# Performance work log

Measured on AMD Instinct MI355X. Metric: run time of the kernel, lower is better.

## Reference

```python
import jax, jax.numpy as jnp
import numpy as np

B, S, D_IN, D_OUT = 4, 4096, 2048, 2048


def setup_inputs() -> dict:
    key = jax.random.key(0)
    kx, kw = jax.random.split(key)
    x = jax.random.normal(kx, (B, S, D_IN), dtype=jnp.float32)
    weight = jax.random.normal(kw, (D_OUT, D_IN), dtype=jnp.float32) * 0.02
    return {"x": x, "weight": weight}


def reference(x, weight):
    # Per-row absmax int8 activation quantization
    x_scale = jnp.clip(jnp.max(jnp.abs(x), axis=-1, keepdims=True), 1e-05, None)  # [B,S,1]
    x_quant = jnp.clip(jnp.round(x / x_scale * 127.0), -128.0, 127.0)
    # Ternary weight quantization (mean-centered absmean scale)
    w_mean = jnp.mean(weight)
    w_centered = weight - w_mean
    w_scale = jnp.clip(jnp.mean(jnp.abs(w_centered)), 1e-05, None)
    w_quant = jnp.clip(jnp.round(w_centered / w_scale), -1.0, 1.0)
    # GEMM on quantized values, then dequant rescale
    y = jnp.einsum('bsi,oi->bso', x_quant, w_quant)  # [B,S,D_OUT]
    y = y * (w_scale * x_scale / 127.0)
    return y.astype(x.dtype)
```

## Files before the change

### kernel.cpp

```cpp
#include <hip/hip_runtime.h>
#include <stdint.h>

#define M_TOT 16384
#define K_DIM 2048
#define N_DIM 2048
#define W_ELEMS (N_DIM * K_DIM)

typedef int v4i __attribute__((ext_vector_type(4)));

__device__ __forceinline__ void async_load16(const void* gptr, void* lptr) {
    __builtin_amdgcn_global_load_lds(
        (__attribute__((address_space(1))) void*)(uintptr_t)gptr,
        (__attribute__((address_space(3))) void*)(uint32_t)(uintptr_t)lptr,
        16, 0, 0);
}

__global__ void wsum_kernel(const float* __restrict__ w, double* __restrict__ sums) {
    int tid = blockIdx.x * 256 + threadIdx.x;
    const float4* w4 = (const float4*)w;
    double s = 0.0;
    for (int i = tid; i < W_ELEMS / 4; i += 512 * 256) {
        float4 v = w4[i];
        s += (double)v.x + (double)v.y + (double)v.z + (double)v.w;
    }
    #pragma unroll
    for (int off = 32; off; off >>= 1) s += __shfl_down(s, off);
    __shared__ double ls[4];
    if ((threadIdx.x & 63) == 0) ls[threadIdx.x >> 6] = s;
    __syncthreads();
    if (threadIdx.x == 0) atomicAdd(&sums[0], ls[0] + ls[1] + ls[2] + ls[3]);
}

__global__ void wabs_kernel(const float* __restrict__ w, double* __restrict__ sums) {
    double mean = sums[0] * (1.0 / (double)W_ELEMS);
    int tid = blockIdx.x * 256 + threadIdx.x;
    const float4* w4 = (const float4*)w;
    double s = 0.0;
    for (int i = tid; i < W_ELEMS / 4; i += 512 * 256) {
        float4 v = w4[i];
        s += fabs((double)v.x - mean) + fabs((double)v.y - mean) +
             fabs((double)v.z - mean) + fabs((double)v.w - mean);
    }
    #pragma unroll
    for (int off = 32; off; off >>= 1) s += __shfl_down(s, off);
    __shared__ double ls[4];
    if ((threadIdx.x & 63) == 0) ls[threadIdx.x >> 6] = s;
    __syncthreads();
    if (threadIdx.x == 0) atomicAdd(&sums[1], ls[0] + ls[1] + ls[2] + ls[3]);
}

__device__ __forceinline__ int qclamp(float v, int lo, int hi) {
    int q = (int)rintf(v);
    q = q > hi ? hi : (q < lo ? lo : q);
    return q & 255;
}

__global__ void wquant_kernel(const float* __restrict__ w, const double* __restrict__ sums,
                              int8_t* __restrict__ wq) {
    float mean  = (float)(sums[0] * (1.0 / (double)W_ELEMS));
    float scale = (float)fmax(sums[1] * (1.0 / (double)W_ELEMS), 1e-5);
    int i = blockIdx.x * 256 + threadIdx.x;
    float4 v = ((const float4*)w)[i];
    int p = qclamp((v.x - mean) / scale, -1, 1)
          | (qclamp((v.y - mean) / scale, -1, 1) << 8)
          | (qclamp((v.z - mean) / scale, -1, 1) << 16)
          | (qclamp((v.w - mean) / scale, -1, 1) << 24);
    ((int*)wq)[i] = p;
}

__global__ __launch_bounds__(256) void xquant_kernel(const float* __restrict__ x,
                                                     int8_t* __restrict__ xq,
                                                     float* __restrict__ xscale) {
    const int row  = (blockIdx.x << 2) | (threadIdx.x >> 6);
    const int lane = threadIdx.x & 63;
    const float4* xr = (const float4*)(x + (size_t)row * K_DIM);
    float4 v[8];
    #pragma unroll
    for (int i = 0; i < 8; i++) v[i] = xr[lane + (i << 6)];
    float m = 0.0f;
    #pragma unroll
    for (int i = 0; i < 8; i++) {
        m = fmaxf(m, fmaxf(fmaxf(fabsf(v[i].x), fabsf(v[i].y)),
                           fmaxf(fabsf(v[i].z), fabsf(v[i].w))));
    }
    #pragma unroll
    for (int off = 32; off; off >>= 1) m = fmaxf(m, __shfl_xor(m, off));
    const float scale = fmaxf(m, 1e-5f);
    if (lane == 0) xscale[row] = scale;
    int* outp = (int*)(xq + (size_t)row * K_DIM);
    #pragma unroll
    for (int i = 0; i < 8; i++) {
        int p = qclamp(v[i].x / scale * 127.0f, -128, 127)
              | (qclamp(v[i].y / scale * 127.0f, -128, 127) << 8)
              | (qclamp(v[i].z / scale * 127.0f, -128, 127) << 16)
              | (qclamp(v[i].w / scale * 127.0f, -128, 127) << 24);
        outp[lane + (i << 6)] = p;
    }
}

__global__ __launch_bounds__(512, 2) void gemm_i8_kernel(
    const int8_t* __restrict__ xq, const int8_t* __restrict__ wq,
    const float* __restrict__ xscale, const double* __restrict__ sums,
    float* __restrict__ out)
{
    __shared__ __align__(16) int8_t lsA[2][32768];
    __shared__ __align__(16) int8_t lsB[2][32768];

    const int tid  = threadIdx.x;
    const int lane = tid & 63;
    const int wv   = tid >> 6;

    const int flat = blockIdx.x;
    const int nf   = ((flat & 7) << 6) | (flat >> 3);
    const int bm   = nf >> 3;
    const int bn   = nf & 7;

    const int sChunk = ((tid & 3) ^ ((tid >> 3) & 3)) << 4;
    const int8_t* gAb = xq + (size_t)(bm * 256 + (tid >> 2)) * K_DIM + sChunk;
    const int8_t* gBb = wq + (size_t)(bn * 256 + (tid >> 2)) * K_DIM + sChunk;
    const int sDst = tid * 16;

    #define STAGE(OP, NB, K0, KH)                                              \
        do {                                                                   \
            async_load16(g##OP##b + (K0) + (KH) * 64,                          \
                         ls##OP[NB] + (KH) * 16384 + sDst);                    \
            async_load16(g##OP##b + (K0) + (KH) * 64 + (size_t)128 * K_DIM,    \
                         ls##OP[NB] + (KH) * 16384 + 8192 + sDst);             \
        } while (0)

    #define VM4 asm volatile("s_waitcnt vmcnt(4)" ::: "memory")
    #define VM0 asm volatile("s_waitcnt vmcnt(0)" ::: "memory")

    const int wm  = (wv >> 2) * 128;
    const int wn  = (wv & 3) * 64;
    const int fr  = lane & 15;
    const int fcl = lane >> 4;
    int aoff[8], boff[4];
    #pragma unroll
    for (int i = 0; i < 8; i++) {
        int ra = wm + i * 16 + fr;
        aoff[i] = ra * 64 + ((fcl ^ ((ra >> 1) & 3)) << 4);
    }
    #pragma unroll
    for (int j = 0; j < 4; j++) {
        int rb = wn + j * 16 + fr;
        boff[j] = rb * 64 + ((fcl ^ ((rb >> 1) & 3)) << 4);
    }

    v4i acc[8][4] = {};
    v4i bf[4];

    #define PHASE(CB, KH, Q, LOADB, EXTRA)                                     \
        do {                                                                   \
            const int8_t* pA_ = lsA[CB] + (KH) * 16384;                        \
            const int8_t* pB_ = lsB[CB] + (KH) * 16384;                        \
            v4i af[4];                                                         \
            _Pragma("unroll")                                                  \
            for (int i_ = 0; i_ < 4; i_++)                                     \
                af[i_] = *(const v4i*)(pA_ + aoff[(Q) * 4 + i_]);              \
            if (LOADB) {                                                       \
                _Pragma("unroll")                                              \
                for (int j_ = 0; j_ < 4; j_++)                                 \
                    bf[j_] = *(const v4i*)(pB_ + boff[j_]);                    \
            }                                                                  \
            EXTRA;                                                             \
            __builtin_amdgcn_s_barrier();                                      \
            __builtin_amdgcn_s_setprio(1);                                     \
            _Pragma("unroll")                                                  \
            for (int i_ = 0; i_ < 4; i_++)                                     \
                _Pragma("unroll")                                              \
                for (int j_ = 0; j_ < 4; j_++)                                 \
                    acc[(Q) * 4 + i_][j_] =                                    \
                        __builtin_amdgcn_mfma_i32_16x16x64_i8(                 \
                            af[i_], bf[j_], acc[(Q) * 4 + i_][j_], 0, 0, 0);   \
            __builtin_amdgcn_s_setprio(0);                                     \
            __builtin_amdgcn_s_barrier();                                      \
        } while (0)

    STAGE(A, 0, 0, 0);
    STAGE(B, 0, 0, 0);
    STAGE(A, 0, 0, 1);
    STAGE(B, 0, 0, 1);
    VM4;
    __builtin_amdgcn_s_barrier();

    for (int t = 0; t < 15; ++t) {
        const int cur = t & 1, nxt = cur ^ 1;
        const int kn = (t + 1) << 7;
        PHASE(cur, 0, 0, true,  STAGE(A, nxt, kn, 0));
        PHASE(cur, 0, 1, false, STAGE(B, nxt, kn, 0); VM4);
        PHASE(cur, 1, 0, true,  STAGE(A, nxt, kn, 1));
        PHASE(cur, 1, 1, false, STAGE(B, nxt, kn, 1); VM4);
    }
    PHASE(1, 0, 0, true,  (void)0);
    PHASE(1, 0, 1, false, VM0);
    PHASE(1, 1, 0, true,  (void)0);
    PHASE(1, 1, 1, false, (void)0);

    #undef PHASE
    #undef STAGE
    #undef VM4
    #undef VM0

    float wscale = (float)fmax(sums[1] * (1.0 / (double)W_ELEMS), 1e-5);
    float f127 = wscale * (1.0f / 127.0f);
    #pragma unroll
    for (int mi = 0; mi < 8; mi++) {
        #pragma unroll
        for (int rg = 0; rg < 4; rg++) {
            int mg = bm * 256 + wm + mi * 16 + (lane >> 4) * 4 + rg;
            float fs = f127 * xscale[mg];
            float* orow = out + (size_t)mg * N_DIM + bn * 256 + wn;
            #pragma unroll
            for (int nj = 0; nj < 4; nj++)
                orow[nj * 16 + fr] = fs * (float)acc[mi][nj][rg];
        }
    }
}

extern "C" void kernel_launch(void* const* d_in, const int* in_sizes, int n_in,
                              void* d_out, int out_size, void* d_ws, size_t ws_size,
                              hipStream_t stream) {
    const float* x = (const float*)d_in[0];
    const float* w = (const float*)d_in[1];
    float* out = (float*)d_out;

    char* ws = (char*)d_ws;
    double* sums   = (double*)ws;
    float*  xscale = (float*)(ws + 64);
    int8_t* xq     = (int8_t*)(ws + 64 + 65536);
    int8_t* wq     = (int8_t*)(ws + 64 + 65536 + (size_t)M_TOT * K_DIM);

    hipMemsetAsync(sums, 0, 16, stream);
    wsum_kernel <<<512, 256, 0, stream>>>(w, sums);
    wabs_kernel <<<512, 256, 0, stream>>>(w, sums);
    wquant_kernel<<<W_ELEMS / 1024, 256, 0, stream>>>(w, sums, wq);
    xquant_kernel<<<M_TOT / 4, 256, 0, stream>>>(x, xq, xscale);
    gemm_i8_kernel<<<dim3(N_DIM / 256 * (M_TOT / 256)), 512, 0, stream>>>(xq, wq, xscale, sums, out);
}
```

Baseline: 322.2 us.

## Shrink GEMM tiles to 128x128, fuse quant kernels, drop memset and atomics

Result: no change. 318.1 us (-1.3%).

```diff
diff --git a/kernel.cpp b/kernel.cpp
--- a/kernel.cpp
+++ b/kernel.cpp
@@ -15,153 +15,170 @@
         16, 0, 0);
 }
 
-__global__ void wsum_kernel(const float* __restrict__ w, double* __restrict__ sums) {
-    int tid = blockIdx.x * 256 + threadIdx.x;
-    const float4* w4 = (const float4*)w;
-    double s = 0.0;
-    for (int i = tid; i < W_ELEMS / 4; i += 512 * 256) {
-        float4 v = w4[i];
-        s += (double)v.x + (double)v.y + (double)v.z + (double)v.w;
-    }
-    #pragma unroll
-    for (int off = 32; off; off >>= 1) s += __shfl_down(s, off);
-    __shared__ double ls[4];
-    if ((threadIdx.x & 63) == 0) ls[threadIdx.x >> 6] = s;
-    __syncthreads();
-    if (threadIdx.x == 0) atomicAdd(&sums[0], ls[0] + ls[1] + ls[2] + ls[3]);
-}
-
-__global__ void wabs_kernel(const float* __restrict__ w, double* __restrict__ sums) {
-    double mean = sums[0] * (1.0 / (double)W_ELEMS);
-    int tid = blockIdx.x * 256 + threadIdx.x;
-    const float4* w4 = (const float4*)w;
-    double s = 0.0;
-    for (int i = tid; i < W_ELEMS / 4; i += 512 * 256) {
-        float4 v = w4[i];
-        s += fabs((double)v.x - mean) + fabs((double)v.y - mean) +
-             fabs((double)v.z - mean) + fabs((double)v.w - mean);
-    }
-    #pragma unroll
-    for (int off = 32; off; off >>= 1) s += __shfl_down(s, off);
-    __shared__ double ls[4];
-    if ((threadIdx.x & 63) == 0) ls[threadIdx.x >> 6] = s;
-    __syncthreads();
-    if (threadIdx.x == 0) atomicAdd(&sums[1], ls[0] + ls[1] + ls[2] + ls[3]);
-}
-
 __device__ __forceinline__ int qclamp(float v, int lo, int hi) {
     int q = (int)rintf(v);
     q = q > hi ? hi : (q < lo ? lo : q);
     return q & 255;
 }
 
-__global__ void wquant_kernel(const float* __restrict__ w, const double* __restrict__ sums,
-                              int8_t* __restrict__ wq) {
-    float mean  = (float)(sums[0] * (1.0 / (double)W_ELEMS));
-    float scale = (float)fmax(sums[1] * (1.0 / (double)W_ELEMS), 1e-5);
-    int i = blockIdx.x * 256 + threadIdx.x;
-    float4 v = ((const float4*)w)[i];
-    int p = qclamp((v.x - mean) / scale, -1, 1)
-          | (qclamp((v.y - mean) / scale, -1, 1) << 8)
-          | (qclamp((v.z - mean) / scale, -1, 1) << 16)
-          | (qclamp((v.w - mean) / scale, -1, 1) << 24);
-    ((int*)wq)[i] = p;
-}
-
-__global__ __launch_bounds__(256) void xquant_kernel(const float* __restrict__ x,
-                                                     int8_t* __restrict__ xq,
-                                                     float* __restrict__ xscale) {
-    const int row  = (blockIdx.x << 2) | (threadIdx.x >> 6);
-    const int lane = threadIdx.x & 63;
-    const float4* xr = (const float4*)(x + (size_t)row * K_DIM);
-    float4 v[8];
-    #pragma unroll
-    for (int i = 0; i < 8; i++) v[i] = xr[lane + (i << 6)];
-    float m = 0.0f;
-    #pragma unroll
-    for (int i = 0; i < 8; i++) {
-        m = fmaxf(m, fmaxf(fmaxf(fabsf(v[i].x), fabsf(v[i].y)),
-                           fmaxf(fabsf(v[i].z), fabsf(v[i].w))));
-    }
-    #pragma unroll
-    for (int off = 32; off; off >>= 1) m = fmaxf(m, __shfl_xor(m, off));
-    const float scale = fmaxf(m, 1e-5f);
-    if (lane == 0) xscale[row] = scale;
-    int* outp = (int*)(xq + (size_t)row * K_DIM);
-    #pragma unroll
-    for (int i = 0; i < 8; i++) {
-        int p = qclamp(v[i].x / scale * 127.0f, -128, 127)
-              | (qclamp(v[i].y / scale * 127.0f, -128, 127) << 8)
-              | (qclamp(v[i].z / scale * 127.0f, -128, 127) << 16)
-              | (qclamp(v[i].w / scale * 127.0f, -128, 127) << 24);
-        outp[lane + (i << 6)] = p;
-    }
-}
-
-__global__ __launch_bounds__(512, 2) void gemm_i8_kernel(
+__global__ __launch_bounds__(256) void wsum_kernel(const float* __restrict__ w,
+                                                   double* __restrict__ spart) {
+    int tid = blockIdx.x * 256 + threadIdx.x;
+    const float4* w4 = (const float4*)w;
+    double s = 0.0;
+    #pragma unroll
+    for (int it = 0; it < 8; it++) {
+        float4 v = w4[tid + it * 131072];
+        s += (double)v.x + (double)v.y + (double)v.z + (double)v.w;
+    }
+    #pragma unroll
+    for (int off = 32; off; off >>= 1) s += __shfl_down(s, off);
+    __shared__ double ls[4];
+    if ((threadIdx.x & 63) == 0) ls[threadIdx.x >> 6] = s;
+    __syncthreads();
+    if (threadIdx.x == 0) spart[blockIdx.x] = ls[0] + ls[1] + ls[2] + ls[3];
+}
+
+__global__ __launch_bounds__(256) void wabs_kernel(const float* __restrict__ w,
+                                                   const double* __restrict__ spart,
+                                                   double* __restrict__ apart) {
+    __shared__ double ls[4];
+    double sm = spart[threadIdx.x] + spart[threadIdx.x + 256];
+    #pragma unroll
+    for (int off = 32; off; off >>= 1) sm += __shfl_down(sm, off);
+    if ((threadIdx.x & 63) == 0) ls[threadIdx.x >> 6] = sm;
+    __syncthreads();
+    double mean = (ls[0] + ls[1] + ls[2] + ls[3]) * (1.0 / (double)W_ELEMS);
+    __syncthreads();
+    int tid = blockIdx.x * 256 + threadIdx.x;
+    const float4* w4 = (const float4*)w;
+    double s = 0.0;
+    #pragma unroll
+    for (int it = 0; it < 8; it++) {
+        float4 v = w4[tid + it * 131072];
+        s += fabs((double)v.x - mean) + fabs((double)v.y - mean) +
+             fabs((double)v.z - mean) + fabs((double)v.w - mean);
+    }
+    #pragma unroll
+    for (int off = 32; off; off >>= 1) s += __shfl_down(s, off);
+    if ((threadIdx.x & 63) == 0) ls[threadIdx.x >> 6] = s;
+    __syncthreads();
+    if (threadIdx.x == 0) apart[blockIdx.x] = ls[0] + ls[1] + ls[2] + ls[3];
+}
+
+__global__ __launch_bounds__(256) void quant_kernel(
+    const float* __restrict__ x, const float* __restrict__ w,
+    const double* __restrict__ spart, const double* __restrict__ apart,
+    int8_t* __restrict__ xq, int8_t* __restrict__ wq,
+    float* __restrict__ xscale, float* __restrict__ wsf)
+{
+    const int t = threadIdx.x;
+    if (blockIdx.x < 4096) {
+        const int row  = (blockIdx.x << 2) | (t >> 6);
+        const int lane = t & 63;
+        const float4* xr = (const float4*)(x + (size_t)row * K_DIM);
+        float4 v[8];
+        #pragma unroll
+        for (int i = 0; i < 8; i++) v[i] = xr[lane + (i << 6)];
+        float m = 0.0f;
+        #pragma unroll
+        for (int i = 0; i < 8; i++)
+            m = fmaxf(m, fmaxf(fmaxf(fabsf(v[i].x), fabsf(v[i].y)),
+                               fmaxf(fabsf(v[i].z), fabsf(v[i].w))));
+        #pragma unroll
+        for (int off = 32; off; off >>= 1) m = fmaxf(m, __shfl_xor(m, off));
+        const float scale = fmaxf(m, 1e-5f);
+        if (lane == 0) xscale[row] = scale;
+        int* outp = (int*)(xq + (size_t)row * K_DIM);
+        #pragma unroll
+        for (int i = 0; i < 8; i++) {
+            int p = qclamp(v[i].x / scale * 127.0f, -128, 127)
+                  | (qclamp(v[i].y / scale * 127.0f, -128, 127) << 8)
+                  | (qclamp(v[i].z / scale * 127.0f, -128, 127) << 16)
+                  | (qclamp(v[i].w / scale * 127.0f, -128, 127) << 24);
+            outp[lane + (i << 6)] = p;
+        }
+    } else {
+        __shared__ double ls0[4], ls1[4];
+        double s0 = spart[t] + spart[t + 256];
+        double s1 = apart[t] + apart[t + 256];
+        #pragma unroll
+        for (int off = 32; off; off >>= 1) {
+            s0 += __shfl_down(s0, off);
+            s1 += __shfl_down(s1, off);
+        }
+        if ((t & 63) == 0) { ls0[t >> 6] = s0; ls1[t >> 6] = s1; }
+        __syncthreads();
+        float mean  = (float)((ls0[0] + ls0[1] + ls0[2] + ls0[3]) * (1.0 / (double)W_ELEMS));
+        float scale = (float)fmax((ls1[0] + ls1[1] + ls1[2] + ls1[3]) * (1.0 / (double)W_ELEMS), 1e-5);
+        int i = (blockIdx.x - 4096) * 256 + t;
+        float4 v = ((const float4*)w)[i];
+        int p = qclamp((v.x - mean) / scale, -1, 1)
+              | (qclamp((v.y - mean) / scale, -1, 1) << 8)
+              | (qclamp((v.z - mean) / scale, -1, 1) << 16)
+              | (qclamp((v.w - mean) / scale, -1, 1) << 24);
+        ((int*)wq)[i] = p;
+        if (i == 0) wsf[0] = scale * (1.0f / 127.0f);
+    }
+}
+
+__global__ __launch_bounds__(256, 2) void gemm_i8_kernel(
     const int8_t* __restrict__ xq, const int8_t* __restrict__ wq,
-    const float* __restrict__ xscale, const double* __restrict__ sums,
+    const float* __restrict__ xscale, const float* __restrict__ wsf,
     float* __restrict__ out)
 {
-    __shared__ __align__(16) int8_t lsA[2][32768];
-    __shared__ __align__(16) int8_t lsB[2][32768];
+    __shared__ __align__(16) int8_t lsA[2][16384];
+    __shared__ __align__(16) int8_t lsB[2][16384];
 
     const int tid  = threadIdx.x;
     const int lane = tid & 63;
     const int wv   = tid >> 6;
 
     const int flat = blockIdx.x;
-    const int nf   = ((flat & 7) << 6) | (flat >> 3);
-    const int bm   = nf >> 3;
-    const int bn   = nf & 7;
+    const int nf   = ((flat & 7) << 8) | (flat >> 3);
+    const int bm   = nf >> 4;
+    const int bn   = nf & 15;
 
     const int sChunk = ((tid & 3) ^ ((tid >> 3) & 3)) << 4;
-    const int8_t* gAb = xq + (size_t)(bm * 256 + (tid >> 2)) * K_DIM + sChunk;
-    const int8_t* gBb = wq + (size_t)(bn * 256 + (tid >> 2)) * K_DIM + sChunk;
+    const int8_t* gAb = xq + (size_t)(bm * 128 + (tid >> 2)) * K_DIM + sChunk;
+    const int8_t* gBb = wq + (size_t)(bn * 128 + (tid >> 2)) * K_DIM + sChunk;
     const int sDst = tid * 16;
 
     #define STAGE(OP, NB, K0, KH)                                              \
         do {                                                                   \
             async_load16(g##OP##b + (K0) + (KH) * 64,                          \
-                         ls##OP[NB] + (KH) * 16384 + sDst);                    \
-            async_load16(g##OP##b + (K0) + (KH) * 64 + (size_t)128 * K_DIM,    \
-                         ls##OP[NB] + (KH) * 16384 + 8192 + sDst);             \
+                         ls##OP[NB] + (KH) * 8192 + sDst);                     \
+            async_load16(g##OP##b + (K0) + (KH) * 64 + (size_t)64 * K_DIM,     \
+                         ls##OP[NB] + (KH) * 8192 + 4096 + sDst);              \
         } while (0)
 
     #define VM4 asm volatile("s_waitcnt vmcnt(4)" ::: "memory")
     #define VM0 asm volatile("s_waitcnt vmcnt(0)" ::: "memory")
 
-    const int wm  = (wv >> 2) * 128;
-    const int wn  = (wv & 3) * 64;
+    const int wm  = (wv >> 1) * 64;
+    const int wn  = (wv & 1) * 64;
     const int fr  = lane & 15;
     const int fcl = lane >> 4;
-    int aoff[8], boff[4];
-    #pragma unroll
-    for (int i = 0; i < 8; i++) {
+    int aoff[4], boff[4];
+    #pragma unroll
+    for (int i = 0; i < 4; i++) {
         int ra = wm + i * 16 + fr;
         aoff[i] = ra * 64 + ((fcl ^ ((ra >> 1) & 3)) << 4);
-    }
-    #pragma unroll
-    for (int j = 0; j < 4; j++) {
-        int rb = wn + j * 16 + fr;
-        boff[j] = rb * 64 + ((fcl ^ ((rb >> 1) & 3)) << 4);
-    }
-
-    v4i acc[8][4] = {};
-    v4i bf[4];
-
-    #define PHASE(CB, KH, Q, LOADB, EXTRA)                                     \
+        int rb = wn + i * 16 + fr;
+        boff[i] = rb * 64 + ((fcl ^ ((rb >> 1) & 3)) << 4);
+    }
+
+    v4i acc[4][4] = {};
+
+    #define PHASE(CB, KH, EXTRA)                                               \
         do {                                                                   \
-            const int8_t* pA_ = lsA[CB] + (KH) * 16384;                        \
-            const int8_t* pB_ = lsB[CB] + (KH) * 16384;                        \
-            v4i af[4];                                                         \
+            const int8_t* pA_ = lsA[CB] + (KH) * 8192;                         \
+            const int8_t* pB_ = lsB[CB] + (KH) * 8192;                         \
+            v4i af[4], bf[4];                                                  \
             _Pragma("unroll")                                                  \
-            for (int i_ = 0; i_ < 4; i_++)                                     \
-                af[i_] = *(const v4i*)(pA_ + aoff[(Q) * 4 + i_]);              \
-            if (LOADB) {                                                       \
-                _Pragma("unroll")                                              \
-                for (int j_ = 0; j_ < 4; j_++)                                 \
-                    bf[j_] = *(const v4i*)(pB_ + boff[j_]);                    \
+            for (int i_ = 0; i_ < 4; i_++) {                                   \
+                af[i_] = *(const v4i*)(pA_ + aoff[i_]);                        \
+                bf[i_] = *(const v4i*)(pB_ + boff[i_]);                        \
             }                                                                  \
             EXTRA;                                                             \
             __builtin_amdgcn_s_barrier();                                      \
@@ -170,9 +187,8 @@
             for (int i_ = 0; i_ < 4; i_++)                                     \
                 _Pragma("unroll")                                              \
                 for (int j_ = 0; j_ < 4; j_++)                                 \
-                    acc[(Q) * 4 + i_][j_] =                                    \
-                        __builtin_amdgcn_mfma_i32_16x16x64_i8(                 \
-                            af[i_], bf[j_], acc[(Q) * 4 + i_][j_], 0, 0, 0);   \
+                    acc[i_][j_] = __builtin_amdgcn_mfma_i32_16x16x64_i8(       \
+                        af[i_], bf[j_], acc[i_][j_], 0, 0, 0);                 \
             __builtin_amdgcn_s_setprio(0);                                     \
             __builtin_amdgcn_s_barrier();                                      \
         } while (0)
@@ -184,33 +200,31 @@
     VM4;
     __builtin_amdgcn_s_barrier();
 
+    #pragma unroll 2
     for (int t = 0; t < 15; ++t) {
         const int cur = t & 1, nxt = cur ^ 1;
         const int kn = (t + 1) << 7;
-        PHASE(cur, 0, 0, true,  STAGE(A, nxt, kn, 0));
-        PHASE(cur, 0, 1, false, STAGE(B, nxt, kn, 0); VM4);
-        PHASE(cur, 1, 0, true,  STAGE(A, nxt, kn, 1));
-        PHASE(cur, 1, 1, false, STAGE(B, nxt, kn, 1); VM4);
-    }
-    PHASE(1, 0, 0, true,  (void)0);
-    PHASE(1, 0, 1, false, VM0);
-    PHASE(1, 1, 0, true,  (void)0);
-    PHASE(1, 1, 1, false, (void)0);
+        PHASE(cur, 0, STAGE(A, nxt, kn, 0); STAGE(B, nxt, kn, 0); VM4);
+        PHASE(cur, 1, STAGE(A, nxt, kn, 1); STAGE(B, nxt, kn, 1); VM4);
+    }
+    PHASE(1, 0, (void)0);
+    VM0;
+    __builtin_amdgcn_s_barrier();
+    PHASE(1, 1, (void)0);
 
     #undef PHASE
     #undef STAGE
     #undef VM4
     #undef VM0
 
-    float wscale = (float)fmax(sums[1] * (1.0 / (double)W_ELEMS), 1e-5);
-    float f127 = wscale * (1.0f / 127.0f);
-    #pragma unroll
-    for (int mi = 0; mi < 8; mi++) {
+    const float f127 = wsf[0];
+    #pragma unroll
+    for (int mi = 0; mi < 4; mi++) {
         #pragma unroll
         for (int rg = 0; rg < 4; rg++) {
-            int mg = bm * 256 + wm + mi * 16 + (lane >> 4) * 4 + rg;
+            int mg = bm * 128 + wm + mi * 16 + (lane >> 4) * 4 + rg;
             float fs = f127 * xscale[mg];
-            float* orow = out + (size_t)mg * N_DIM + bn * 256 + wn;
+            float* orow = out + (size_t)mg * N_DIM + bn * 128 + wn;
             #pragma unroll
             for (int nj = 0; nj < 4; nj++)
                 orow[nj * 16 + fr] = fs * (float)acc[mi][nj][rg];
@@ -226,15 +240,15 @@
     float* out = (float*)d_out;
 
     char* ws = (char*)d_ws;
-    double* sums   = (double*)ws;
-    float*  xscale = (float*)(ws + 64);
-    int8_t* xq     = (int8_t*)(ws + 64 + 65536);
-    int8_t* wq     = (int8_t*)(ws + 64 + 65536 + (size_t)M_TOT * K_DIM);
-
-    hipMemsetAsync(sums, 0, 16, stream);
-    wsum_kernel <<<512, 256, 0, stream>>>(w, sums);
-    wabs_kernel <<<512, 256, 0, stream>>>(w, sums);
-    wquant_kernel<<<W_ELEMS / 1024, 256, 0, stream>>>(w, sums, wq);
-    xquant_kernel<<<M_TOT / 4, 256, 0, stream>>>(x, xq, xscale);
-    gemm_i8_kernel<<<dim3(N_DIM / 256 * (M_TOT / 256)), 512, 0, stream>>>(xq, wq, xscale, sums, out);
-}
+    double* spart  = (double*)ws;
+    double* apart  = (double*)(ws + 4096);
+    float*  wsf    = (float*)(ws + 8192);
+    float*  xscale = (float*)(ws + 12288);
+    int8_t* xq     = (int8_t*)(ws + 12288 + 65536);
+    int8_t* wq     = xq + (size_t)M_TOT * K_DIM;
+
+    wsum_kernel <<<512, 256, 0, stream>>>(w, spart);
+    wabs_kernel <<<512, 256, 0, stream>>>(w, spart, apart);
+    quant_kernel<<<8192, 256, 0, stream>>>(x, w, spart, apart, xq, wq, xscale, wsf);
+    gemm_i8_kernel<<<2048, 256, 0, stream>>>(xq, wq, xscale, wsf, out);
+}
```
